# Optimization experiments

Measured on AMD Instinct MI355X. Metric: run time of the kernel, lower is better.

## Reference

```python
import jax, jax.numpy as jnp
import numpy as np

B, L, D = 64, 196, 512      # batch, num annotation vectors, encoder_dim
A, M, N = 512, 512, 512     # attention_dim, embed_dim, decoder_dim
K, T_MAX = 10000, 32        # vocab_size, max caption length


def setup_inputs() -> dict:
    key = jax.random.key(0)
    ks = jax.random.split(key, 32)
    sc = 0.02

    def w(i, shape):
        return jax.random.normal(ks[i], shape, jnp.float32) * sc

    lens = jnp.sort(jax.random.randint(ks[2], (B,), 2, T_MAX + 1))[::-1]
    lens = lens.at[0].set(T_MAX)  # sorted descending; ensures max_decode_len = T_MAX-1

    return {
        "encoder_out": jax.random.normal(ks[0], (B, L, D), jnp.float32),
        "captions": jax.random.randint(ks[1], (B, T_MAX), 0, K),
        "caption_lengths": lens,
        # embedding (uniform(-0.1, 0.1) per _init_weights)
        "emb": jax.random.uniform(ks[3], (K, M), jnp.float32, -0.1, 0.1),
        # attention MLP (Show-Attend-Tell style: relu then scalar projection)
        "W_ea": w(4, (D, A)), "b_ea": jnp.zeros((A,), jnp.float32),
        "W_da": w(5, (N, A)), "b_da": jnp.zeros((A,), jnp.float32),
        "w_fa": w(6, (A,)),   "b_fa": jnp.zeros((), jnp.float32),
        # init_h / init_c
        "W_hi": w(7, (D, N)), "b_hi": jnp.zeros((N,), jnp.float32),
        "W_ci": w(8, (D, N)), "b_ci": jnp.zeros((N,), jnp.float32),
        # LSTMCell (PyTorch gate order i, f, g, o along 4N)
        "W_ih": w(9, (M + D, 4 * N)), "W_hh": w(10, (N, 4 * N)),
        "b_ih": jnp.zeros((4 * N,), jnp.float32), "b_hh": jnp.zeros((4 * N,), jnp.float32),
        # f_beta gate
        "W_fb": w(11, (N, D)), "b_fb": jnp.zeros((D,), jnp.float32),
        # deep output layers
        "W_lh": w(12, (N, M)), "b_lh": jnp.zeros((M,), jnp.float32),
        "W_lz": w(13, (D, M)), "b_lz": jnp.zeros((M,), jnp.float32),
        "W_lo": jax.random.uniform(ks[14], (M, K), jnp.float32, -0.1, 0.1),
        "b_lo": jnp.zeros((K,), jnp.float32),
    }


def reference(encoder_out, captions, caption_lengths, emb,
              W_ea, b_ea, W_da, b_da, w_fa, b_fa,
              W_hi, b_hi, W_ci, b_ci,
              W_ih, W_hh, b_ih, b_hh,
              W_fb, b_fb, W_lh, b_lh, W_lz, b_lz, W_lo, b_lo):
    # dropout is evaluated in eval mode (identity)
    T = captions.shape[1] - 1                 # max_decode_len (lengths sorted desc, max = T_MAX)
    dec_len = caption_lengths - 1             # (B,)

    mean_ann = encoder_out.mean(axis=1)       # (B, D)
    h0 = jnp.tanh(mean_ann @ W_hi + b_hi)
    c0 = jnp.tanh(mean_ann @ W_ci + b_ci)

    embs = emb[captions]                      # (B, T_MAX, M)
    emb_seq = jnp.swapaxes(embs[:, :T], 0, 1) # (T, B, M)
    att1 = encoder_out @ W_ea + b_ea          # (B, L, A) precomputed once

    def step(carry, xs):
        h, c = carry
        t, emb_t = xs
        # soft attention
        att2 = h @ W_da + b_da                              # (B, A)
        e = jax.nn.relu(att1 + att2[:, None, :]) @ w_fa + b_fa  # (B, L)
        alpha = jax.nn.softmax(e, axis=-1)
        z = jnp.einsum('bl,bld->bd', alpha, encoder_out)    # (B, D)
        beta = jax.nn.sigmoid(h @ W_fb + b_fb)
        z = beta * z
        # LSTM cell
        x = jnp.concatenate([emb_t, z], axis=1)             # (B, M+D)
        gates = x @ W_ih + h @ W_hh + b_ih + b_hh
        i, f, g, o = jnp.split(gates, 4, axis=1)
        c_new = jax.nn.sigmoid(f) * c + jax.nn.sigmoid(i) * jnp.tanh(g)
        h_new = jax.nn.sigmoid(o) * jnp.tanh(c_new)
        # deep output
        logits = (emb_t + h_new @ W_lh + b_lh + z @ W_lz + b_lz) @ W_lo + b_lo
        # ragged mask: only sequences with dec_len > t are active (emulates h[:batch_size_t])
        m = t < dec_len                                     # (B,)
        mf = m[:, None].astype(h.dtype)
        h = jnp.where(m[:, None], h_new, h)
        c = jnp.where(m[:, None], c_new, c)
        return (h, c), (logits * mf, alpha * mf)

    _, (preds, alphas) = jax.lax.scan(step, (h0, c0), (jnp.arange(T), emb_seq))
    predictions = jnp.swapaxes(preds, 0, 1)   # (B, T, K)
    alphas_out = jnp.swapaxes(alphas, 0, 1)   # (B, T, L)
    return predictions, alphas_out
```

## Files before the change

### kernel.cpp

```cpp
#include <hip/hip_runtime.h>
#include <hip/hip_bf16.h>
#include <hip/hip_cooperative_groups.h>

namespace cg = cooperative_groups;

typedef short short8 __attribute__((ext_vector_type(8)));
typedef float floatx4 __attribute__((ext_vector_type(4)));
typedef _Float16 h2v __attribute__((ext_vector_type(2)));

#define B_ 64
#define L_ 196
#define T_ 31
#define PRED_ 19840000ULL

__device__ __forceinline__ float bf2f(unsigned short u){
  union { unsigned int i; float f; } v; v.i = ((unsigned int)u)<<16; return v.f;
}
__device__ __forceinline__ unsigned short bfu(float x){
  union { __hip_bfloat16 h; unsigned short u; } v; v.h = __float2bfloat16(x); return v.u;
}
__device__ __forceinline__ unsigned int pk2(float a, float b){
  return (unsigned int)bfu(a) | ((unsigned int)bfu(b) << 16);
}
__device__ __forceinline__ unsigned int pkh2(float a, float b){
  union { _Float16 h[2]; unsigned int u; } v;
  v.h[0] = (_Float16)a; v.h[1] = (_Float16)b; return v.u;
}
__device__ __forceinline__ float sigm(float x){ return 1.0f/(1.0f+__expf(-x)); }

__device__ __forceinline__ float dot2(unsigned int a, unsigned int b, float c){
#if __has_builtin(__builtin_amdgcn_fdot2)
  return __builtin_amdgcn_fdot2(__builtin_bit_cast(h2v, a), __builtin_bit_cast(h2v, b), c, false);
#else
  union { unsigned int u; _Float16 h[2]; } x, y; x.u = a; y.u = b;
  return c + (float)x.h[0]*(float)y.h[0] + (float)x.h[1]*(float)y.h[1];
#endif
}

__global__ __launch_bounds__(256) void k_cast(const float* __restrict__ src,
                                              __hip_bfloat16* __restrict__ dst, int n4){
  int i = blockIdx.x*256 + threadIdx.x;
  if (i < n4){
    const float4 v = *(const float4*)(src + (size_t)i*4);
    size_t o = (size_t)i*4;
    dst[o+0] = __float2bfloat16(v.x);
    dst[o+1] = __float2bfloat16(v.y);
    dst[o+2] = __float2bfloat16(v.z);
    dst[o+3] = __float2bfloat16(v.w);
  }
}

__global__ __launch_bounds__(1024) void k_trans_bf16(const float* __restrict__ src,
    __hip_bfloat16* __restrict__ dst, int Kin, int Nin, int S, int Rtot){
  __shared__ float tile[32][33];
  int n0 = blockIdx.x*32, k0 = blockIdx.y*32;
  int x = threadIdx.x & 31, y = threadIdx.x >> 5;
  int k = k0 + y, nn = n0 + x;
  tile[y][x] = (k < Kin && nn < Nin) ? src[(size_t)k*Nin + nn] : 0.0f;
  __syncthreads();
  int n2 = n0 + y, k2 = k0 + x;
  if (n2 < Rtot && k2 < Kin) dst[(size_t)n2*S + k2] = __float2bfloat16(tile[x][y]);
}

__global__ __launch_bounds__(1024) void k_trans_f16(const float* __restrict__ src,
    _Float16* __restrict__ dst, int Kin, int Nin, int S, int Rtot){
  __shared__ float tile[32][33];
  int n0 = blockIdx.x*32, k0 = blockIdx.y*32;
  int x = threadIdx.x & 31, y = threadIdx.x >> 5;
  int k = k0 + y, nn = n0 + x;
  tile[y][x] = (k < Kin && nn < Nin) ? src[(size_t)k*Nin + nn] : 0.0f;
  __syncthreads();
  int n2 = n0 + y, k2 = k0 + x;
  if (n2 < Rtot && k2 < Kin) dst[(size_t)n2*S + k2] = (_Float16)tile[x][y];
}

__global__ __launch_bounds__(512) void k_emb(const int* __restrict__ captions,
    const float* __restrict__ emb, __hip_bfloat16* __restrict__ Erow){
  int tb = blockIdx.x; int t = tb >> 6; int b = tb & 63; int m = threadIdx.x;
  int cap = captions[b*32 + t];
  Erow[((size_t)(t*64 + b))*512 + m] = __float2bfloat16(emb[(size_t)cap*512 + m]);
}

__global__ __launch_bounds__(512) void k_init(const float* __restrict__ enc,
    const float* __restrict__ Whi, const float* __restrict__ bhi,
    const float* __restrict__ Wci, const float* __restrict__ bci,
    float* __restrict__ hT, float* __restrict__ cT, unsigned int* __restrict__ hP){
  int b = blockIdx.x; int d = threadIdx.x;
  __shared__ float ms[512];
  __shared__ float hs[512];
  const float* eb = enc + (size_t)b*L_*512;
  float s = 0.f;
  for (int l = 0; l < L_; l++) s += eb[(size_t)l*512 + d];
  ms[d] = s * (1.0f/196.0f);
  __syncthreads();
  float a1 = bhi[d], a2 = bci[d];
  #pragma unroll 4
  for (int k = 0; k < 512; k++){
    float mv = ms[k];
    a1 += mv * Whi[(size_t)k*512 + d];
    a2 += mv * Wci[(size_t)k*512 + d];
  }
  float h = tanhf(a1);
  hT[d*64 + b] = h;
  cT[d*64 + b] = tanhf(a2);
  hs[d] = h;
  __syncthreads();
  if (d < 256) hP[d*64 + b] = pkh2(hs[2*d], hs[2*d+1]);
}

__global__ __launch_bounds__(256) void k_gemm(const __hip_bfloat16* __restrict__ Abf,
    const __hip_bfloat16* __restrict__ Bt, int K, int mode, int Nreal,
    const float* __restrict__ bias1, const float* __restrict__ bias2,
    const __hip_bfloat16* __restrict__ Erow, const int* __restrict__ caplen,
    __hip_bfloat16* __restrict__ outB, float* __restrict__ outF){
  int bx = blockIdx.x, by = blockIdx.y;
  if (mode == 2){
    int i = bx; int xcd = i & 7; int ii = i >> 3;
    int s = (xcd < 3) ? xcd*609 + ii : 3*609 + (xcd-3)*608 + ii;
    by = s % 31;
    bx = s / 31;
  }
  int lane = threadIdx.x & 63; int wv = threadIdx.x >> 6;
  int wr = wv >> 1, wc = wv & 1;
  int r0 = by*64 + wr*32;
  int c0 = bx*64 + wc*32;
  int l15 = lane & 15, lg = lane >> 4;
  const short* Ap = (const short*)Abf;
  const short* Bp = (const short*)Bt;
  floatx4 acc00 = {0,0,0,0}, acc01 = {0,0,0,0}, acc10 = {0,0,0,0}, acc11 = {0,0,0,0};
  size_t ar0 = (size_t)(r0 + l15)*K + lg*8;
  size_t ar1 = ar0 + (size_t)16*K;
  size_t br0 = (size_t)(c0 + l15)*K + lg*8;
  size_t br1 = br0 + (size_t)16*K;
  #pragma unroll 4
  for (int k0 = 0; k0 < K; k0 += 32){
    short8 av0 = *(const short8*)(Ap + ar0 + k0);
    short8 av1 = *(const short8*)(Ap + ar1 + k0);
    short8 bv0 = *(const short8*)(Bp + br0 + k0);
    short8 bv1 = *(const short8*)(Bp + br1 + k0);
    acc00 = __builtin_amdgcn_mfma_f32_16x16x32_bf16(av0, bv0, acc00, 0, 0, 0);
    acc01 = __builtin_amdgcn_mfma_f32_16x16x32_bf16(av0, bv1, acc01, 0, 0, 0);
    acc10 = __builtin_amdgcn_mfma_f32_16x16x32_bf16(av1, bv0, acc10, 0, 0, 0);
    acc11 = __builtin_amdgcn_mfma_f32_16x16x32_bf16(av1, bv1, acc11, 0, 0, 0);
  }
  floatx4 accs[2][2] = {{acc00, acc01}, {acc10, acc11}};
  #pragma unroll
  for (int i = 0; i < 2; i++){
    #pragma unroll
    for (int j = 0; j < 2; j++){
      #pragma unroll
      for (int v = 0; v < 4; v++){
        int r = r0 + 16*i + lg*4 + v;
        int c = c0 + 16*j + l15;
        float val = accs[i][j][v];
        if (mode == 0){
          outB[(size_t)r*512 + c] = __float2bfloat16(val + bias1[c]);
        } else if (mode == 1){
          float e = bf2f(((const unsigned short*)Erow)[(size_t)r*512 + c]);
          outB[(size_t)r*512 + c] = __float2bfloat16(val + bias1[c] + bias2[c] + e);
        } else if (mode == 2){
          if (c < Nreal){
            int t = r >> 6, b = r & 63;
            float mf = (t < caplen[b] - 1) ? 1.f : 0.f;
            outF[((size_t)b*T_ + t)*10000 + c] = (val + bias1[c]) * mf;
          }
        } else {
          outB[((size_t)(r >> 6)*2048 + c)*64 + (r & 63)] = __float2bfloat16(val);
        }
      }
    }
  }
}

__global__ __launch_bounds__(1024, 4) void k_loop(
    const unsigned int* __restrict__ W1h,
    const unsigned int* __restrict__ Wzh,
    const __hip_bfloat16* __restrict__ preIH,
    const __hip_bfloat16* __restrict__ att1R,
    const __hip_bfloat16* __restrict__ enc_bf,
    const float* __restrict__ wfa,
    const float* __restrict__ b_da, const float* __restrict__ b_fb,
    const float* __restrict__ b_ih, const float* __restrict__ b_hh,
    const float* __restrict__ hT0, const float* __restrict__ cT0,
    unsigned int* __restrict__ hP,
    unsigned int* __restrict__ zP,
    float* __restrict__ att2g,
    float* __restrict__ betag,
    __hip_bfloat16* __restrict__ HZ,
    const int* __restrict__ caplen,
    float* __restrict__ outAlpha)
{
  cg::grid_group grid = cg::this_grid();
  int tid = threadIdx.x, lane = tid & 63, w = tid >> 6;
  int blk = blockIdx.x;

  __shared__ unsigned int wA_l[12][256];
  __shared__ unsigned int wZ_l[8][256];
  __shared__ float wfa_l[512];
  __shared__ float whh_l[8][64];
  __shared__ float hst[2][64], cst[2][64];
  __shared__ float bsum_l[8];
  __shared__ float biasAB_l[4];
  __shared__ float scr[6144];
  __shared__ float es[196], ps[196], att2s[512], zsc[512], MS[1];
  __shared__ float glds[8][64];

  for (int i = tid; i < 3072; i += 1024){
    int ra = i >> 8, kp = i & 255;
    int row;
    if (ra < 4) row = blk*4 + ra;
    else { int rc = ra - 4; row = 1024 + (rc >> 1)*512 + blk*2 + (rc & 1); }
    wA_l[ra][kp] = W1h[(size_t)row*256 + kp];
  }
  for (int i = tid; i < 2048; i += 1024){
    int rc = i >> 8, kp = i & 255;
    int row = (rc >> 1)*512 + blk*2 + (rc & 1);
    wZ_l[rc][kp] = Wzh[(size_t)row*256 + kp];
  }
  for (int i = tid; i < 512; i += 1024) wfa_l[i] = wfa[i];
  if (tid < 128){ int j = tid >> 6;
    hst[j][lane] = hT0[(blk*2+j)*64 + lane];
    cst[j][lane] = cT0[(blk*2+j)*64 + lane];
  }
  if (tid < 8){ int g = tid >> 1, j = tid & 1;
    bsum_l[tid] = b_ih[g*512 + blk*2 + j] + b_hh[g*512 + blk*2 + j];
  }
  if (tid < 4){ int ab = blk*4 + tid;
    biasAB_l[tid] = (ab < 512) ? b_da[ab] : b_fb[ab - 512];
  }
  int dl  = caplen[lane] - 1;
  int dlb = (blk < 64) ? (caplen[blk] - 1) : 0;
  __syncthreads();

  for (int t = 0; t < T_; t++){
    {
      int half = w >> 3, kc = w & 7;
      unsigned int hv[32];
      const unsigned int* hp = hP + kc*32*64 + lane;
      #pragma unroll
      for (int i = 0; i < 32; i++) hv[i] = hp[i*64];
      float acc[6] = {0,0,0,0,0,0};
      #pragma unroll
      for (int i = 0; i < 32; i++){
        unsigned int h = hv[i];
        #pragma unroll
        for (int r = 0; r < 6; r++)
          acc[r] = dot2(wA_l[half*6 + r][kc*32 + i], h, acc[r]);
      }
      #pragma unroll
      for (int r = 0; r < 6; r++) scr[((half*6 + r)*8 + kc)*64 + lane] = acc[r];
    }
    __syncthreads();
    if (tid < 768){
      int r = tid >> 6, b = tid & 63;
      float s = 0.f;
      #pragma unroll
      for (int kc = 0; kc < 8; kc++) s += scr[(r*8 + kc)*64 + b];
      if (r < 4){
        int ab = blk*4 + r;
        float v = s + biasAB_l[r];
        if (ab < 512) att2g[ab*64 + b] = v;
        else          betag[(ab-512)*64 + b] = v;
      } else {
        whh_l[r-4][b] = s;
      }
    }
    grid.sync();

    if (blk < 64){
      if (tid < 512){ att2s[tid] = att2g[tid*64 + blk]; zsc[tid] = 0.f; }
      __syncthreads();
      {
        float a2r[8], wfr[8];
        #pragma unroll
        for (int u = 0; u < 8; u++){ a2r[u] = att2s[lane*8+u]; wfr[u] = wfa_l[lane*8+u]; }
        #pragma unroll
        for (int i = 0; i < 13; i++){
          int l = w + i*16; int lc = (l < 196) ? l : 195;
          short8 av = *(const short8*)((const short*)att1R + ((size_t)(blk*196 + lc))*512 + lane*8);
          if (l < 196){
            float e = 0.f;
            #pragma unroll
            for (int u = 0; u < 8; u++){
              float v = bf2f((unsigned short)av[u]) + a2r[u];
              v = fmaxf(v, 0.f);
              e += v * wfr[u];
            }
            #pragma unroll
            for (int off = 32; off; off >>= 1) e += __shfl_xor(e, off, 64);
            if (lane == 0) es[l] = e;
          }
        }
      }
      __syncthreads();
      if (w == 0){
        float v0 = es[lane], v1 = es[lane+64], v2 = es[lane+128];
        float v3 = (lane < 4) ? es[lane+192] : -3e38f;
        float m = fmaxf(fmaxf(v0,v1), fmaxf(v2,v3));
        #pragma unroll
        for (int off = 32; off; off >>= 1) m = fmaxf(m, __shfl_xor(m, off, 64));
        float p0 = __expf(v0-m), p1 = __expf(v1-m), p2 = __expf(v2-m);
        float p3 = (lane < 4) ? __expf(v3-m) : 0.f;
        float s = p0+p1+p2+p3;
        #pragma unroll
        for (int off = 32; off; off >>= 1) s += __shfl_xor(s, off, 64);
        ps[lane] = p0; ps[lane+64] = p1; ps[lane+128] = p2;
        if (lane < 4) ps[lane+192] = p3;
        if (lane == 0) MS[0] = 1.f / s;
      }
      __syncthreads();
      float inv = MS[0];
      if (tid < 196){
        float mf = (t < dlb) ? 1.f : 0.f;
        outAlpha[((size_t)blk*T_ + t)*196 + tid] = ps[tid] * inv * mf;
      }
      {
        float zac[8] = {0,0,0,0,0,0,0,0};
        #pragma unroll
        for (int i = 0; i < 13; i++){
          int l = w + i*16; int lc = (l < 196) ? l : 195;
          short8 ev = *(const short8*)((const short*)enc_bf + ((size_t)(blk*196 + lc))*512 + lane*8);
          float pl = (l < 196) ? ps[l] : 0.f;
          #pragma unroll
          for (int u = 0; u < 8; u++) zac[u] += pl * bf2f((unsigned short)ev[u]);
        }
        #pragma unroll
        for (int u = 0; u < 8; u++) atomicAdd(&zsc[lane*8 + u], zac[u]);
      }
      __syncthreads();
      if (tid < 256){
        int d0 = tid*2;
        float za = zsc[d0]   * inv * sigm(betag[(size_t)d0*64 + blk]);
        float zb = zsc[d0+1] * inv * sigm(betag[(size_t)(d0+1)*64 + blk]);
        zP[tid*64 + blk] = pkh2(za, zb);
        *(unsigned int*)((unsigned short*)HZ + ((size_t)(t*64 + blk))*1024 + 512 + d0) = pk2(za, zb);
      }
    }
    grid.sync();

    {
      int half = w >> 3, kc = w & 7;
      unsigned int zv[32];
      const unsigned int* zp = zP + kc*32*64 + lane;
      #pragma unroll
      for (int i = 0; i < 32; i++) zv[i] = zp[i*64];
      float acc[4] = {0,0,0,0};
      #pragma unroll
      for (int i = 0; i < 32; i++){
        unsigned int z = zv[i];
        #pragma unroll
        for (int r = 0; r < 4; r++)
          acc[r] = dot2(wZ_l[half*4 + r][kc*32 + i], z, acc[r]);
      }
      #pragma unroll
      for (int r = 0; r < 4; r++) scr[((half*4 + r)*8 + kc)*64 + lane] = acc[r];
    }
    __syncthreads();
    if (tid < 512){
      int rc = tid >> 6, b = tid & 63;
      int g = rc >> 1, j = rc & 1;
      float s = 0.f;
      #pragma unroll
      for (int kc = 0; kc < 8; kc++) s += scr[(rc*8 + kc)*64 + b];
      s += whh_l[rc][b] + bsum_l[rc]
         + bf2f(((const unsigned short*)preIH)[((size_t)t*2048 + g*512 + blk*2 + j)*64 + b]);
      glds[rc][b] = s;
    }
    __syncthreads();
    if (tid < 64){
      int b = tid;
      float hm2[2];
      #pragma unroll
      for (int j = 0; j < 2; j++){
        float gi = glds[0 + j][b], gf = glds[2 + j][b];
        float gg = glds[4 + j][b], go = glds[6 + j][b];
        float c_old = cst[j][b];
        float c_new = sigm(gf)*c_old + sigm(gi)*tanhf(gg);
        float h_new = sigm(go)*tanhf(c_new);
        bool mm = (t < dl);
        float hm = mm ? h_new : hst[j][b];
        cst[j][b] = mm ? c_new : c_old;
        hst[j][b] = hm;
        hm2[j] = hm;
        ((unsigned short*)HZ)[((size_t)(t*64 + b))*1024 + blk*2 + j] = bfu(h_new);
      }
      hP[blk*64 + b] = pkh2(hm2[0], hm2[1]);
    }
    grid.sync();
  }
}

extern "C" void kernel_launch(void* const* d_in, const int* in_sizes, int n_in,
                              void* d_out, int out_size, void* d_ws, size_t ws_size,
                              hipStream_t stream){
  (void)in_sizes; (void)n_in; (void)out_size; (void)ws_size;
  const float* enc    = (const float*)d_in[0];
  const int* captions = (const int*)d_in[1];
  const int* caplen   = (const int*)d_in[2];
  const float* emb    = (const float*)d_in[3];
  const float* W_ea  = (const float*)d_in[4];  const float* b_ea = (const float*)d_in[5];
  const float* W_da  = (const float*)d_in[6];  const float* b_da = (const float*)d_in[7];
  const float* w_fa  = (const float*)d_in[8];
  const float* W_hi  = (const float*)d_in[10]; const float* b_hi = (const float*)d_in[11];
  const float* W_ci  = (const float*)d_in[12]; const float* b_ci = (const float*)d_in[13];
  const float* W_ih  = (const float*)d_in[14]; const float* W_hh = (const float*)d_in[15];
  const float* b_ih  = (const float*)d_in[16]; const float* b_hh = (const float*)d_in[17];
  const float* W_fb  = (const float*)d_in[18]; const float* b_fb = (const float*)d_in[19];
  const float* W_lh  = (const float*)d_in[20]; const float* b_lh = (const float*)d_in[21];
  const float* W_lz  = (const float*)d_in[22]; const float* b_lz = (const float*)d_in[23];
  const float* W_lo  = (const float*)d_in[24]; const float* b_lo = (const float*)d_in[25];
  float* out = (float*)d_out;

  char* p = (char*)d_ws;
  auto alloc = [&](size_t bytes){ char* r = p; p += (bytes + 255) & ~(size_t)255; return r; };
  __hip_bfloat16* enc_bf = (__hip_bfloat16*)alloc(12845056);
  __hip_bfloat16* att1R  = (__hip_bfloat16*)alloc(12845056);
  __hip_bfloat16* WeaT   = (__hip_bfloat16*)alloc(524288);
  _Float16*       W1h    = (_Float16*)alloc(3145728);
  _Float16*       Wzh    = (_Float16*)alloc(2097152);
  __hip_bfloat16* WtopT  = (__hip_bfloat16*)alloc(2097152);
  __hip_bfloat16* W2T    = (__hip_bfloat16*)alloc(1048576);
  __hip_bfloat16* WloT   = (__hip_bfloat16*)alloc(10289152);
  __hip_bfloat16* Erow   = (__hip_bfloat16*)alloc(2031616);
  __hip_bfloat16* preIH  = (__hip_bfloat16*)alloc(8126464);
  __hip_bfloat16* HZ     = (__hip_bfloat16*)alloc(4063232);
  __hip_bfloat16* Ubf    = (__hip_bfloat16*)alloc(2031616);
  float*        hT0    = (float*)alloc(131072);
  float*        cT0    = (float*)alloc(131072);
  unsigned int* hP     = (unsigned int*)alloc(65536);
  unsigned int* zP     = (unsigned int*)alloc(65536);
  float*        att2g  = (float*)alloc(131072);
  float*        betag  = (float*)alloc(131072);

  k_cast<<<dim3(6272), dim3(256), 0, stream>>>(enc, enc_bf, 1605632);
  k_trans_f16<<<dim3(16, 16), dim3(1024), 0, stream>>>(W_da, W1h,            512, 512,  512, 512);
  k_trans_f16<<<dim3(16, 16), dim3(1024), 0, stream>>>(W_fb, W1h + 512*512,  512, 512,  512, 512);
  k_trans_f16<<<dim3(64, 16), dim3(1024), 0, stream>>>(W_hh, W1h + 1024*512, 512, 2048, 512, 2048);
  k_trans_f16<<<dim3(64, 16), dim3(1024), 0, stream>>>(W_ih + 512*2048, Wzh, 512, 2048, 512, 2048);
  k_trans_bf16<<<dim3(16, 16), dim3(1024), 0, stream>>>(W_ea, WeaT,      512, 512,   512,  512);
  k_trans_bf16<<<dim3(64, 16), dim3(1024), 0, stream>>>(W_ih, WtopT,     512, 2048,  512,  2048);
  k_trans_bf16<<<dim3(16, 16), dim3(1024), 0, stream>>>(W_lh, W2T,       512, 512,   1024, 512);
  k_trans_bf16<<<dim3(16, 16), dim3(1024), 0, stream>>>(W_lz, W2T + 512, 512, 512,   1024, 512);
  k_trans_bf16<<<dim3(314, 16), dim3(1024), 0, stream>>>(W_lo, WloT,     512, 10000, 512,  10048);
  k_emb<<<dim3(1984), dim3(512), 0, stream>>>(captions, emb, Erow);
  k_init<<<dim3(64), dim3(512), 0, stream>>>(enc, W_hi, b_hi, W_ci, b_ci, hT0, cT0, hP);

  k_gemm<<<dim3(8, 196), dim3(256), 0, stream>>>(enc_bf, WeaT, 512, 0, 512,
      b_ea, nullptr, nullptr, nullptr, att1R, nullptr);
  k_gemm<<<dim3(32, 31), dim3(256), 0, stream>>>(Erow, WtopT, 512, 3, 2048,
      nullptr, nullptr, nullptr, nullptr, preIH, nullptr);

  {
    const unsigned int *a0 = (const unsigned int*)W1h, *a1 = (const unsigned int*)Wzh;
    const __hip_bfloat16 *a2 = preIH, *a3 = att1R, *a4 = enc_bf;
    const float *f0 = w_fa, *f1 = b_da, *f2 = b_fb, *f3 = b_ih, *f4 = b_hh, *f5 = hT0, *f6 = cT0;
    unsigned int *u0 = hP, *u1 = zP;
    float *g0 = att2g, *g1 = betag;
    __hip_bfloat16 *hz = HZ;
    const int* cl = caplen;
    float* oa = out + PRED_;
    void* args[] = { &a0,&a1,&a2,&a3,&a4, &f0,&f1,&f2,&f3,&f4,&f5,&f6,
                     &u0,&u1, &g0,&g1, &hz, &cl, &oa };
    hipLaunchCooperativeKernel((const void*)k_loop, dim3(256), dim3(1024), args, 0, stream);
  }

  k_gemm<<<dim3(8, 31), dim3(256), 0, stream>>>(HZ, W2T, 1024, 1, 512,
      b_lh, b_lz, Erow, nullptr, Ubf, nullptr);
  k_gemm<<<dim3(4867), dim3(256), 0, stream>>>(Ubf, WloT, 512, 2, 10000,
      b_lo, nullptr, nullptr, caplen, nullptr, out);
}
```

Measured before the change: 4.601 ms.

## Replace cooperative grid-synced LSTM loop with independent per-batch blocks

The recurrent kernel becomes a plain launch of 64 blocks, one per batch row, with no grid-wide barriers. Each block now computes every output feature itself and reads the packed f16 weights (W_da/W_fb/W_hh and W_ih's z part) from global memory on every timestep. The h and z state stays in shared memory instead of passing through global memory. New pack kernels and a batch-major preIH layout support this. It removes three grid syncs per step, but it gives up the weights held in shared memory, uses only 64 CUs, and makes each block stream several MB from cache on every step.

```diff
diff --git a/kernel.cpp b/kernel.cpp
--- a/kernel.cpp
+++ b/kernel.cpp
@@ -1,8 +1,5 @@
 #include <hip/hip_runtime.h>
 #include <hip/hip_bf16.h>
-#include <hip/hip_cooperative_groups.h>
-
-namespace cg = cooperative_groups;
 
 typedef short short8 __attribute__((ext_vector_type(8)));
 typedef float floatx4 __attribute__((ext_vector_type(4)));
@@ -62,16 +59,23 @@
   if (n2 < Rtot && k2 < Kin) dst[(size_t)n2*S + k2] = __float2bfloat16(tile[x][y]);
 }
 
-__global__ __launch_bounds__(1024) void k_trans_f16(const float* __restrict__ src,
-    _Float16* __restrict__ dst, int Kin, int Nin, int S, int Rtot){
-  __shared__ float tile[32][33];
-  int n0 = blockIdx.x*32, k0 = blockIdx.y*32;
-  int x = threadIdx.x & 31, y = threadIdx.x >> 5;
-  int k = k0 + y, nn = n0 + x;
-  tile[y][x] = (k < Kin && nn < Nin) ? src[(size_t)k*Nin + nn] : 0.0f;
-  __syncthreads();
-  int n2 = n0 + y, k2 = k0 + x;
-  if (n2 < Rtot && k2 < Kin) dst[(size_t)n2*S + k2] = (_Float16)tile[x][y];
+__global__ __launch_bounds__(1024) void k_pack1(const float* __restrict__ Wda,
+    const float* __restrict__ Wfb, const float* __restrict__ Whh,
+    unsigned int* __restrict__ W1p){
+  int kp = blockIdx.y; int n = blockIdx.x*1024 + threadIdx.x;
+  float v0, v1;
+  if (n < 512){       v0 = Wda[(size_t)(2*kp)*512 + n];        v1 = Wda[(size_t)(2*kp+1)*512 + n]; }
+  else if (n < 1024){ v0 = Wfb[(size_t)(2*kp)*512 + n-512];    v1 = Wfb[(size_t)(2*kp+1)*512 + n-512]; }
+  else {              v0 = Whh[(size_t)(2*kp)*2048 + n-1024];  v1 = Whh[(size_t)(2*kp+1)*2048 + n-1024]; }
+  W1p[(size_t)kp*3072 + n] = pkh2(v0, v1);
+}
+
+__global__ __launch_bounds__(1024) void k_pack2(const float* __restrict__ Wih,
+    unsigned int* __restrict__ W2p){
+  int kp = blockIdx.y; int n = blockIdx.x*1024 + threadIdx.x;
+  float v0 = Wih[(size_t)(512 + 2*kp)*2048 + n];
+  float v1 = Wih[(size_t)(513 + 2*kp)*2048 + n];
+  W2p[(size_t)kp*2048 + n] = pkh2(v0, v1);
 }
 
 __global__ __launch_bounds__(512) void k_emb(const int* __restrict__ captions,
@@ -84,10 +88,9 @@
 __global__ __launch_bounds__(512) void k_init(const float* __restrict__ enc,
     const float* __restrict__ Whi, const float* __restrict__ bhi,
     const float* __restrict__ Wci, const float* __restrict__ bci,
-    float* __restrict__ hT, float* __restrict__ cT, unsigned int* __restrict__ hP){
+    float* __restrict__ hb0, float* __restrict__ cb0){
   int b = blockIdx.x; int d = threadIdx.x;
   __shared__ float ms[512];
-  __shared__ float hs[512];
   const float* eb = enc + (size_t)b*L_*512;
   float s = 0.f;
   for (int l = 0; l < L_; l++) s += eb[(size_t)l*512 + d];
@@ -100,12 +103,8 @@
     a1 += mv * Whi[(size_t)k*512 + d];
     a2 += mv * Wci[(size_t)k*512 + d];
   }
-  float h = tanhf(a1);
-  hT[d*64 + b] = h;
-  cT[d*64 + b] = tanhf(a2);
-  hs[d] = h;
-  __syncthreads();
-  if (d < 256) hP[d*64 + b] = pkh2(hs[2*d], hs[2*d+1]);
+  hb0[(size_t)b*512 + d] = tanhf(a1);
+  cb0[(size_t)b*512 + d] = tanhf(a2);
 }
 
 __global__ __launch_bounds__(256) void k_gemm(const __hip_bfloat16* __restrict__ Abf,
@@ -165,228 +164,175 @@
             outF[((size_t)b*T_ + t)*10000 + c] = (val + bias1[c]) * mf;
           }
         } else {
-          outB[((size_t)(r >> 6)*2048 + c)*64 + (r & 63)] = __float2bfloat16(val);
+          outB[((size_t)(r & 63)*T_ + (r >> 6))*2048 + c] = __float2bfloat16(val);
         }
       }
     }
   }
 }
 
-__global__ __launch_bounds__(1024, 4) void k_loop(
-    const unsigned int* __restrict__ W1h,
-    const unsigned int* __restrict__ Wzh,
-    const __hip_bfloat16* __restrict__ preIH,
+__global__ __launch_bounds__(1024) void k_loop(
+    const unsigned int* __restrict__ W1p,
+    const unsigned int* __restrict__ W2p,
+    const __hip_bfloat16* __restrict__ preIHb,
     const __hip_bfloat16* __restrict__ att1R,
     const __hip_bfloat16* __restrict__ enc_bf,
     const float* __restrict__ wfa,
     const float* __restrict__ b_da, const float* __restrict__ b_fb,
     const float* __restrict__ b_ih, const float* __restrict__ b_hh,
-    const float* __restrict__ hT0, const float* __restrict__ cT0,
-    unsigned int* __restrict__ hP,
-    unsigned int* __restrict__ zP,
-    float* __restrict__ att2g,
-    float* __restrict__ betag,
+    const float* __restrict__ hb0, const float* __restrict__ cb0,
     __hip_bfloat16* __restrict__ HZ,
     const int* __restrict__ caplen,
     float* __restrict__ outAlpha)
 {
-  cg::grid_group grid = cg::this_grid();
   int tid = threadIdx.x, lane = tid & 63, w = tid >> 6;
-  int blk = blockIdx.x;
-
-  __shared__ unsigned int wA_l[12][256];
-  __shared__ unsigned int wZ_l[8][256];
+  int b = blockIdx.x;
+
+  __shared__ unsigned int hpk[256];
+  __shared__ unsigned int zpk[256];
+  __shared__ float hs[512], cs[512];
+  __shared__ float att2s[512], betas[512];
+  __shared__ float es[196], ps[196];
+  __shared__ float zsc[512];
+  __shared__ float gfo[2][512];
   __shared__ float wfa_l[512];
-  __shared__ float whh_l[8][64];
-  __shared__ float hst[2][64], cst[2][64];
-  __shared__ float bsum_l[8];
-  __shared__ float biasAB_l[4];
-  __shared__ float scr[6144];
-  __shared__ float es[196], ps[196], att2s[512], zsc[512], MS[1];
-  __shared__ float glds[8][64];
-
-  for (int i = tid; i < 3072; i += 1024){
-    int ra = i >> 8, kp = i & 255;
-    int row;
-    if (ra < 4) row = blk*4 + ra;
-    else { int rc = ra - 4; row = 1024 + (rc >> 1)*512 + blk*2 + (rc & 1); }
-    wA_l[ra][kp] = W1h[(size_t)row*256 + kp];
-  }
-  for (int i = tid; i < 2048; i += 1024){
-    int rc = i >> 8, kp = i & 255;
-    int row = (rc >> 1)*512 + blk*2 + (rc & 1);
-    wZ_l[rc][kp] = Wzh[(size_t)row*256 + kp];
-  }
-  for (int i = tid; i < 512; i += 1024) wfa_l[i] = wfa[i];
-  if (tid < 128){ int j = tid >> 6;
-    hst[j][lane] = hT0[(blk*2+j)*64 + lane];
-    cst[j][lane] = cT0[(blk*2+j)*64 + lane];
-  }
-  if (tid < 8){ int g = tid >> 1, j = tid & 1;
-    bsum_l[tid] = b_ih[g*512 + blk*2 + j] + b_hh[g*512 + blk*2 + j];
-  }
-  if (tid < 4){ int ab = blk*4 + tid;
-    biasAB_l[tid] = (ab < 512) ? b_da[ab] : b_fb[ab - 512];
-  }
-  int dl  = caplen[lane] - 1;
-  int dlb = (blk < 64) ? (caplen[blk] - 1) : 0;
+  __shared__ float MS[1];
+
+  if (tid < 512){
+    hs[tid] = hb0[(size_t)b*512 + tid];
+    cs[tid] = cb0[(size_t)b*512 + tid];
+    wfa_l[tid] = wfa[tid];
+  }
   __syncthreads();
+  if (tid < 256) hpk[tid] = pkh2(hs[2*tid], hs[2*tid+1]);
+  float biasA = (tid < 512) ? b_da[tid] : b_fb[tid - 512];
+  float bs0 = b_ih[tid]        + b_hh[tid];
+  float bs1 = b_ih[1024 + tid] + b_hh[1024 + tid];
+  int dl = caplen[b] - 1;
+  __syncthreads();
 
   for (int t = 0; t < T_; t++){
+    float a0 = 0.f, a1 = 0.f, a2 = 0.f;
     {
-      int half = w >> 3, kc = w & 7;
-      unsigned int hv[32];
-      const unsigned int* hp = hP + kc*32*64 + lane;
-      #pragma unroll
-      for (int i = 0; i < 32; i++) hv[i] = hp[i*64];
-      float acc[6] = {0,0,0,0,0,0};
-      #pragma unroll
-      for (int i = 0; i < 32; i++){
-        unsigned int h = hv[i];
-        #pragma unroll
-        for (int r = 0; r < 6; r++)
-          acc[r] = dot2(wA_l[half*6 + r][kc*32 + i], h, acc[r]);
+      const unsigned int* wp = W1p + tid;
+      #pragma unroll 4
+      for (int kp = 0; kp < 256; kp++){
+        unsigned int hh = hpk[kp];
+        a0 = dot2(wp[0],    hh, a0);
+        a1 = dot2(wp[1024], hh, a1);
+        a2 = dot2(wp[2048], hh, a2);
+        wp += 3072;
       }
-      #pragma unroll
-      for (int r = 0; r < 6; r++) scr[((half*6 + r)*8 + kc)*64 + lane] = acc[r];
-    }
-    __syncthreads();
-    if (tid < 768){
-      int r = tid >> 6, b = tid & 63;
-      float s = 0.f;
-      #pragma unroll
-      for (int kc = 0; kc < 8; kc++) s += scr[(r*8 + kc)*64 + b];
-      if (r < 4){
-        int ab = blk*4 + r;
-        float v = s + biasAB_l[r];
-        if (ab < 512) att2g[ab*64 + b] = v;
-        else          betag[(ab-512)*64 + b] = v;
-      } else {
-        whh_l[r-4][b] = s;
-      }
-    }
-    grid.sync();
-
-    if (blk < 64){
-      if (tid < 512){ att2s[tid] = att2g[tid*64 + blk]; zsc[tid] = 0.f; }
-      __syncthreads();
-      {
-        float a2r[8], wfr[8];
-        #pragma unroll
-        for (int u = 0; u < 8; u++){ a2r[u] = att2s[lane*8+u]; wfr[u] = wfa_l[lane*8+u]; }
-        #pragma unroll
-        for (int i = 0; i < 13; i++){
-          int l = w + i*16; int lc = (l < 196) ? l : 195;
-          short8 av = *(const short8*)((const short*)att1R + ((size_t)(blk*196 + lc))*512 + lane*8);
-          if (l < 196){
-            float e = 0.f;
-            #pragma unroll
-            for (int u = 0; u < 8; u++){
-              float v = bf2f((unsigned short)av[u]) + a2r[u];
-              v = fmaxf(v, 0.f);
-              e += v * wfr[u];
-            }
-            #pragma unroll
-            for (int off = 32; off; off >>= 1) e += __shfl_xor(e, off, 64);
-            if (lane == 0) es[l] = e;
+    }
+    if (tid < 512) att2s[tid] = a0 + biasA;
+    else           betas[tid - 512] = a0 + biasA;
+    if (tid < 512) zsc[tid] = 0.f;
+    __syncthreads();
+
+    {
+      float a2r[8], wfr[8];
+      #pragma unroll
+      for (int u = 0; u < 8; u++){ a2r[u] = att2s[lane*8+u]; wfr[u] = wfa_l[lane*8+u]; }
+      #pragma unroll
+      for (int i = 0; i < 13; i++){
+        int l = w + i*16;
+        if (l < 196){
+          short8 av = *(const short8*)((const short*)att1R + ((size_t)(b*196 + l))*512 + lane*8);
+          float e = 0.f;
+          #pragma unroll
+          for (int u = 0; u < 8; u++){
+            float v = bf2f((unsigned short)av[u]) + a2r[u];
+            e += fmaxf(v, 0.f) * wfr[u];
           }
+          #pragma unroll
+          for (int off = 32; off; off >>= 1) e += __shfl_xor(e, off, 64);
+          if (lane == 0) es[l] = e;
         }
       }
-      __syncthreads();
-      if (w == 0){
-        float v0 = es[lane], v1 = es[lane+64], v2 = es[lane+128];
-        float v3 = (lane < 4) ? es[lane+192] : -3e38f;
-        float m = fmaxf(fmaxf(v0,v1), fmaxf(v2,v3));
+    }
+    __syncthreads();
+
+    if (w == 0){
+      float v0 = es[lane], v1 = es[lane+64], v2 = es[lane+128];
+      float v3 = (lane < 4) ? es[lane+192] : -3e38f;
+      float m = fmaxf(fmaxf(v0,v1), fmaxf(v2,v3));
+      #pragma unroll
+      for (int off = 32; off; off >>= 1) m = fmaxf(m, __shfl_xor(m, off, 64));
+      float p0 = __expf(v0-m), p1 = __expf(v1-m), p2 = __expf(v2-m);
+      float p3 = (lane < 4) ? __expf(v3-m) : 0.f;
+      float s = p0+p1+p2+p3;
+      #pragma unroll
+      for (int off = 32; off; off >>= 1) s += __shfl_xor(s, off, 64);
+      ps[lane] = p0; ps[lane+64] = p1; ps[lane+128] = p2;
+      if (lane < 4) ps[lane+192] = p3;
+      if (lane == 0) MS[0] = 1.f / s;
+    }
+    __syncthreads();
+    float inv = MS[0];
+    if (tid < 196){
+      float mf = (t < dl) ? 1.f : 0.f;
+      outAlpha[((size_t)b*T_ + t)*196 + tid] = ps[tid] * inv * mf;
+    }
+
+    {
+      float zac[8] = {0,0,0,0,0,0,0,0};
+      #pragma unroll
+      for (int i = 0; i < 13; i++){
+        int l = w + i*16; int lc = (l < 196) ? l : 195;
+        short8 ev = *(const short8*)((const short*)enc_bf + ((size_t)(b*196 + lc))*512 + lane*8);
+        float pl = (l < 196) ? ps[l] : 0.f;
         #pragma unroll
-        for (int off = 32; off; off >>= 1) m = fmaxf(m, __shfl_xor(m, off, 64));
-        float p0 = __expf(v0-m), p1 = __expf(v1-m), p2 = __expf(v2-m);
-        float p3 = (lane < 4) ? __expf(v3-m) : 0.f;
-        float s = p0+p1+p2+p3;
-        #pragma unroll
-        for (int off = 32; off; off >>= 1) s += __shfl_xor(s, off, 64);
-        ps[lane] = p0; ps[lane+64] = p1; ps[lane+128] = p2;
-        if (lane < 4) ps[lane+192] = p3;
-        if (lane == 0) MS[0] = 1.f / s;
+        for (int u = 0; u < 8; u++) zac[u] += pl * bf2f((unsigned short)ev[u]);
       }
-      __syncthreads();
-      float inv = MS[0];
-      if (tid < 196){
-        float mf = (t < dlb) ? 1.f : 0.f;
-        outAlpha[((size_t)blk*T_ + t)*196 + tid] = ps[tid] * inv * mf;
+      #pragma unroll
+      for (int u = 0; u < 8; u++) atomicAdd(&zsc[lane*8 + u], zac[u]);
+    }
+    __syncthreads();
+
+    if (tid < 256){
+      int d0 = tid*2;
+      float za = zsc[d0]   * inv * sigm(betas[d0]);
+      float zb = zsc[d0+1] * inv * sigm(betas[d0+1]);
+      zpk[tid] = pkh2(za, zb);
+      *(unsigned int*)((unsigned short*)HZ + ((size_t)(t*64 + b))*1024 + 512 + d0) = pk2(za, zb);
+    }
+    __syncthreads();
+
+    float g0 = a1 + bs0;
+    float g1 = a2 + bs1;
+    {
+      const unsigned int* wp = W2p + tid;
+      #pragma unroll 4
+      for (int kp = 0; kp < 256; kp++){
+        unsigned int zz = zpk[kp];
+        g0 = dot2(wp[0],    zz, g0);
+        g1 = dot2(wp[1024], zz, g1);
+        wp += 2048;
       }
-      {
-        float zac[8] = {0,0,0,0,0,0,0,0};
-        #pragma unroll
-        for (int i = 0; i < 13; i++){
-          int l = w + i*16; int lc = (l < 196) ? l : 195;
-          short8 ev = *(const short8*)((const short*)enc_bf + ((size_t)(blk*196 + lc))*512 + lane*8);
-          float pl = (l < 196) ? ps[l] : 0.f;
-          #pragma unroll
-          for (int u = 0; u < 8; u++) zac[u] += pl * bf2f((unsigned short)ev[u]);
-        }
-        #pragma unroll
-        for (int u = 0; u < 8; u++) atomicAdd(&zsc[lane*8 + u], zac[u]);
-      }
-      __syncthreads();
-      if (tid < 256){
-        int d0 = tid*2;
-        float za = zsc[d0]   * inv * sigm(betag[(size_t)d0*64 + blk]);
-        float zb = zsc[d0+1] * inv * sigm(betag[(size_t)(d0+1)*64 + blk]);
-        zP[tid*64 + blk] = pkh2(za, zb);
-        *(unsigned int*)((unsigned short*)HZ + ((size_t)(t*64 + blk))*1024 + 512 + d0) = pk2(za, zb);
-      }
-    }
-    grid.sync();
-
+    }
     {
-      int half = w >> 3, kc = w & 7;
-      unsigned int zv[32];
-      const unsigned int* zp = zP + kc*32*64 + lane;
-      #pragma unroll
-      for (int i = 0; i < 32; i++) zv[i] = zp[i*64];
-      float acc[4] = {0,0,0,0};
-      #pragma unroll
-      for (int i = 0; i < 32; i++){
-        unsigned int z = zv[i];
-        #pragma unroll
-        for (int r = 0; r < 4; r++)
-          acc[r] = dot2(wZ_l[half*4 + r][kc*32 + i], z, acc[r]);
-      }
-      #pragma unroll
-      for (int r = 0; r < 4; r++) scr[((half*4 + r)*8 + kc)*64 + lane] = acc[r];
-    }
-    __syncthreads();
+      const unsigned short* pre = (const unsigned short*)preIHb + ((size_t)b*T_ + t)*2048;
+      g0 += bf2f(pre[tid]);
+      g1 += bf2f(pre[1024 + tid]);
+    }
+    if (tid >= 512){ gfo[0][tid-512] = g0; gfo[1][tid-512] = g1; }
+    __syncthreads();
+
     if (tid < 512){
-      int rc = tid >> 6, b = tid & 63;
-      int g = rc >> 1, j = rc & 1;
-      float s = 0.f;
-      #pragma unroll
-      for (int kc = 0; kc < 8; kc++) s += scr[(rc*8 + kc)*64 + b];
-      s += whh_l[rc][b] + bsum_l[rc]
-         + bf2f(((const unsigned short*)preIH)[((size_t)t*2048 + g*512 + blk*2 + j)*64 + b]);
-      glds[rc][b] = s;
-    }
-    __syncthreads();
-    if (tid < 64){
-      int b = tid;
-      float hm2[2];
-      #pragma unroll
-      for (int j = 0; j < 2; j++){
-        float gi = glds[0 + j][b], gf = glds[2 + j][b];
-        float gg = glds[4 + j][b], go = glds[6 + j][b];
-        float c_old = cst[j][b];
-        float c_new = sigm(gf)*c_old + sigm(gi)*tanhf(gg);
-        float h_new = sigm(go)*tanhf(c_new);
-        bool mm = (t < dl);
-        float hm = mm ? h_new : hst[j][b];
-        cst[j][b] = mm ? c_new : c_old;
-        hst[j][b] = hm;
-        hm2[j] = hm;
-        ((unsigned short*)HZ)[((size_t)(t*64 + b))*1024 + blk*2 + j] = bfu(h_new);
-      }
-      hP[blk*64 + b] = pkh2(hm2[0], hm2[1]);
-    }
-    grid.sync();
+      float gi = g0, gg = g1;
+      float gf = gfo[0][tid], go = gfo[1][tid];
+      float c_old = cs[tid];
+      float c_new = sigm(gf)*c_old + sigm(gi)*tanhf(gg);
+      float h_new = sigm(go)*tanhf(c_new);
+      bool mm = (t < dl);
+      float hm = mm ? h_new : hs[tid];
+      cs[tid] = mm ? c_new : c_old;
+      hs[tid] = hm;
+      ((unsigned short*)HZ)[((size_t)(t*64 + b))*1024 + tid] = bfu(h_new);
+    }
+    __syncthreads();
+    if (tid < 256) hpk[tid] = pkh2(hs[2*tid], hs[2*tid+1]);
+    __syncthreads();
   }
 }
 
@@ -416,53 +362,36 @@
   __hip_bfloat16* enc_bf = (__hip_bfloat16*)alloc(12845056);
   __hip_bfloat16* att1R  = (__hip_bfloat16*)alloc(12845056);
   __hip_bfloat16* WeaT   = (__hip_bfloat16*)alloc(524288);
-  _Float16*       W1h    = (_Float16*)alloc(3145728);
-  _Float16*       Wzh    = (_Float16*)alloc(2097152);
+  unsigned int*   W1p    = (unsigned int*)alloc(3145728);
+  unsigned int*   W2p    = (unsigned int*)alloc(2097152);
   __hip_bfloat16* WtopT  = (__hip_bfloat16*)alloc(2097152);
   __hip_bfloat16* W2T    = (__hip_bfloat16*)alloc(1048576);
   __hip_bfloat16* WloT   = (__hip_bfloat16*)alloc(10289152);
   __hip_bfloat16* Erow   = (__hip_bfloat16*)alloc(2031616);
-  __hip_bfloat16* preIH  = (__hip_bfloat16*)alloc(8126464);
+  __hip_bfloat16* preIHb = (__hip_bfloat16*)alloc(8126464);
   __hip_bfloat16* HZ     = (__hip_bfloat16*)alloc(4063232);
   __hip_bfloat16* Ubf    = (__hip_bfloat16*)alloc(2031616);
-  float*        hT0    = (float*)alloc(131072);
-  float*        cT0    = (float*)alloc(131072);
-  unsigned int* hP     = (unsigned int*)alloc(65536);
-  unsigned int* zP     = (unsigned int*)alloc(65536);
-  float*        att2g  = (float*)alloc(131072);
-  float*        betag  = (float*)alloc(131072);
+  float*        hb0    = (float*)alloc(131072);
+  float*        cb0    = (float*)alloc(131072);
 
   k_cast<<<dim3(6272), dim3(256), 0, stream>>>(enc, enc_bf, 1605632);
-  k_trans_f16<<<dim3(16, 16), dim3(1024), 0, stream>>>(W_da, W1h,            512, 512,  512, 512);
-  k_trans_f16<<<dim3(16, 16), dim3(1024), 0, stream>>>(W_fb, W1h + 512*512,  512, 512,  512, 512);
-  k_trans_f16<<<dim3(64, 16), dim3(1024), 0, stream>>>(W_hh, W1h + 1024*512, 512, 2048, 512, 2048);
-  k_trans_f16<<<dim3(64, 16), dim3(1024), 0, stream>>>(W_ih + 512*2048, Wzh, 512, 2048, 512, 2048);
+  k_pack1<<<dim3(3, 256), dim3(1024), 0, stream>>>(W_da, W_fb, W_hh, W1p);
+  k_pack2<<<dim3(2, 256), dim3(1024), 0, stream>>>(W_ih, W2p);
   k_trans_bf16<<<dim3(16, 16), dim3(1024), 0, stream>>>(W_ea, WeaT,      512, 512,   512,  512);
   k_trans_bf16<<<dim3(64, 16), dim3(1024), 0, stream>>>(W_ih, WtopT,     512, 2048,  512,  2048);
   k_trans_bf16<<<dim3(16, 16), dim3(1024), 0, stream>>>(W_lh, W2T,       512, 512,   1024, 512);
   k_trans_bf16<<<dim3(16, 16), dim3(1024), 0, stream>>>(W_lz, W2T + 512, 512, 512,   1024, 512);
   k_trans_bf16<<<dim3(314, 16), dim3(1024), 0, stream>>>(W_lo, WloT,     512, 10000, 512,  10048);
   k_emb<<<dim3(1984), dim3(512), 0, stream>>>(captions, emb, Erow);
-  k_init<<<dim3(64), dim3(512), 0, stream>>>(enc, W_hi, b_hi, W_ci, b_ci, hT0, cT0, hP);
+  k_init<<<dim3(64), dim3(512), 0, stream>>>(enc, W_hi, b_hi, W_ci, b_ci, hb0, cb0);
 
   k_gemm<<<dim3(8, 196), dim3(256), 0, stream>>>(enc_bf, WeaT, 512, 0, 512,
       b_ea, nullptr, nullptr, nullptr, att1R, nullptr);
   k_gemm<<<dim3(32, 31), dim3(256), 0, stream>>>(Erow, WtopT, 512, 3, 2048,
-      nullptr, nullptr, nullptr, nullptr, preIH, nullptr);
-
-  {
-    const unsigned int *a0 = (const unsigned int*)W1h, *a1 = (const unsigned int*)Wzh;
-    const __hip_bfloat16 *a2 = preIH, *a3 = att1R, *a4 = enc_bf;
-    const float *f0 = w_fa, *f1 = b_da, *f2 = b_fb, *f3 = b_ih, *f4 = b_hh, *f5 = hT0, *f6 = cT0;
-    unsigned int *u0 = hP, *u1 = zP;
-    float *g0 = att2g, *g1 = betag;
-    __hip_bfloat16 *hz = HZ;
-    const int* cl = caplen;
-    float* oa = out + PRED_;
-    void* args[] = { &a0,&a1,&a2,&a3,&a4, &f0,&f1,&f2,&f3,&f4,&f5,&f6,
-                     &u0,&u1, &g0,&g1, &hz, &cl, &oa };
-    hipLaunchCooperativeKernel((const void*)k_loop, dim3(256), dim3(1024), args, 0, stream);
-  }
+      nullptr, nullptr, nullptr, nullptr, preIHb, nullptr);
+
+  k_loop<<<dim3(64), dim3(1024), 0, stream>>>(W1p, W2p, preIHb, att1R, enc_bf,
+      w_fa, b_da, b_fb, b_ih, b_hh, hb0, cb0, HZ, caplen, out + PRED_);
 
   k_gemm<<<dim3(8, 31), dim3(256), 0, stream>>>(HZ, W2T, 1024, 1, 512,
       b_lh, b_lz, Erow, nullptr, Ubf, nullptr);
```

After: 11.47 ms. 149% more time.
